# Performance work log

Hardware: AMD Instinct MI355X
Metric: run time of the kernel (lower is better)

Reference implementation:

```python
import jax, jax.numpy as jnp
import numpy as np

B, K, DA, DZ, H = 8, 256, 64, 32, 128
DIR_IN = 2 * DA + 5 + 4 * DZ  # 261
NONE_IN = 5 + 2 * DA + 4 * DZ  # 261
HUGE = 1000000.0


def _init_mlp(key, d_in, h):
    k1, k2, k3 = jax.random.split(key, 3)
    s1 = 1.0 / np.sqrt(d_in)
    s2 = 1.0 / np.sqrt(h)
    return (
        jax.random.uniform(k1, (d_in, h), jnp.float32, -s1, s1), jnp.zeros((h,), jnp.float32),
        jax.random.uniform(k2, (h, h), jnp.float32, -s2, s2), jnp.zeros((h,), jnp.float32),
        jax.random.uniform(k3, (h, 1), jnp.float32, -s2, s2), jnp.zeros((1,), jnp.float32),
    )


def setup_inputs() -> dict:
    key = jax.random.key(0)
    ks = jax.random.split(key, 5)
    agent_feat = jax.random.normal(ks[0], (B, K, DA), jnp.float32)
    z_mean = jax.random.normal(ks[1], (B, K, DZ), jnp.float32)
    z_logvar = jax.random.normal(ks[2], (B, K, DZ), jnp.float32)
    agent_mask = jnp.ones((B, K), jnp.float32)
    W1d, b1d, W2d, b2d, W3d, b3d = _init_mlp(ks[3], DIR_IN, H)
    W1n, b1n, W2n, b2n, W3n, b3n = _init_mlp(ks[4], NONE_IN, H)
    return dict(agent_feat=agent_feat, z_mean=z_mean, z_logvar=z_logvar,
                agent_mask=agent_mask,
                W1d=W1d, b1d=b1d, W2d=W2d, b2d=b2d, W3d=W3d, b3d=b3d,
                W1n=W1n, b1n=b1n, W2n=W2n, b2n=b2n, W3n=W3n, b3n=b3n)


def _mlp(x, W1, b1, W2, b2, W3, b3):
    h = jax.nn.relu(jnp.einsum('bijf,fh->bijh', x, W1) + b1)
    h = jax.nn.relu(jnp.einsum('bijh,hg->bijg', h, W2) + b2)
    return (jnp.einsum('bijh,ho->bijo', h, W3) + b3)[..., 0]  # [B,K,K]


def reference(agent_feat, z_mean, z_logvar, agent_mask,
              W1d, b1d, W2d, b2d, W3d, b3d,
              W1n, b1n, W2n, b2n, W3n, b3n):
    Bv, Kv, Da = agent_feat.shape
    ai = jnp.broadcast_to(agent_feat[:, :, None, :], (Bv, Kv, Kv, Da))
    aj = jnp.broadcast_to(agent_feat[:, None, :, :], (Bv, Kv, Kv, Da))
    Dz = z_mean.shape[-1]
    zi_m = jnp.broadcast_to(z_mean[:, :, None, :], (Bv, Kv, Kv, Dz))
    zj_m = jnp.broadcast_to(z_mean[:, None, :, :], (Bv, Kv, Kv, Dz))
    zi_lv = jnp.broadcast_to(z_logvar[:, :, None, :], (Bv, Kv, Kv, Dz))
    zj_lv = jnp.broadcast_to(z_logvar[:, None, :, :], (Bv, Kv, Kv, Dz))
    rel_pos = aj[..., 0:2] - ai[..., 0:2]
    rel_vel = aj[..., 3:5] - ai[..., 3:5]
    dist = jnp.linalg.norm(rel_pos, axis=-1, keepdims=True)
    geom = jnp.concatenate([rel_pos, rel_vel, dist], axis=-1)  # [B,K,K,5]
    dir_feat = jnp.concatenate([ai, aj, geom, zi_m, zi_lv, zj_m, zj_lv], axis=-1)
    none_feat = jnp.concatenate([geom, ai, aj, zi_m, zi_lv, zj_m, zj_lv], axis=-1)

    e_dir = _mlp(dir_feat, W1d, b1d, W2d, b2d, W3d, b3d)
    e_none = _mlp(none_feat, W1n, b1n, W2n, b2n, W3n, b3n)

    pair_mask = agent_mask[:, :, None] * agent_mask[:, None, :]
    pair_mask = pair_mask * (1.0 - jnp.eye(Kv, dtype=agent_feat.dtype)[None])
    keep = pair_mask > 0.5
    e_dir = jnp.where(keep, e_dir, HUGE)
    e_none = jnp.where(keep, e_none, HUGE)
    e_none = 0.5 * (e_none + jnp.swapaxes(e_none, 1, 2))
    return e_dir, e_none
```

## Files before the change

### kernel.cpp

```cpp
#include <hip/hip_runtime.h>

typedef unsigned short u16;
typedef unsigned int u32;
typedef short s16x8 __attribute__((ext_vector_type(8)));
typedef float f32x4 __attribute__((ext_vector_type(4)));
typedef u32 u32x4 __attribute__((ext_vector_type(4)));

#define UT_D   0u
#define VT_D   524288u
#define UT_N   1048576u
#define VT_N   1572864u
#define W2T_D  2097152u
#define W2T_N  2129920u
#define ERAW   2162688u

__device__ __forceinline__ u16 f2bf(float x) {
  u32 u = __float_as_uint(x);
  return (u16)((u + 0x7FFFu + ((u >> 16) & 1u)) >> 16);
}
__device__ __forceinline__ u32 cvt_pk_bf16(float lo, float hi) {
  u32 r;
  asm("v_cvt_pk_bf16_f32 %0, %1, %2" : "=v"(r) : "v"(lo), "v"(hi));
  return r;
}
__device__ __forceinline__ s16x8 as_frag(u32x4 v) { return __builtin_bit_cast(s16x8, v); }

__global__ __launch_bounds__(256) void k_uv(
    const float* __restrict__ af, const float* __restrict__ zm, const float* __restrict__ zlv,
    const float* __restrict__ W1d, const float* __restrict__ b1d,
    const float* __restrict__ W1n, const float* __restrict__ b1n,
    u16* __restrict__ ws16) {
  const int a0  = blockIdx.x * 8;
  const int mlp = blockIdx.y;
  const int t   = threadIdx.x;
  __shared__ float xs[8][128];
  for (int idx = t; idx < 1024; idx += 256) {
    const int a = idx >> 7, f = idx & 127, ga = a0 + a;
    float v;
    if (f < 64)      v = af[ga*64 + f];
    else if (f < 96) v = zm[ga*32 + (f-64)];
    else             v = zlv[ga*32 + (f-96)];
    xs[a][f] = v;
  }
  __syncthreads();
  const int h = t & 127, half = t >> 7;
  const float* W1 = mlp ? W1n : W1d;
  const int aoff = (mlp ? 5 : 0) + 64*half;
  const int zoff = 69 + 64*half;
  float acc[8];
  #pragma unroll
  for (int a = 0; a < 8; ++a) acc[a] = 0.f;
  #pragma unroll 2
  for (int f = 0; f < 64; f += 4) {
    const float w0 = W1[(aoff+f  )*128 + h];
    const float w1 = W1[(aoff+f+1)*128 + h];
    const float w2 = W1[(aoff+f+2)*128 + h];
    const float w3 = W1[(aoff+f+3)*128 + h];
    #pragma unroll
    for (int a = 0; a < 8; ++a) {
      const f32x4 xv = *(const f32x4*)&xs[a][f];
      acc[a] = fmaf(xv[3], w3, fmaf(xv[2], w2, fmaf(xv[1], w1, fmaf(xv[0], w0, acc[a]))));
    }
  }
  #pragma unroll 2
  for (int f = 64; f < 128; f += 4) {
    const float w0 = W1[(zoff+f  )*128 + h];
    const float w1 = W1[(zoff+f+1)*128 + h];
    const float w2 = W1[(zoff+f+2)*128 + h];
    const float w3 = W1[(zoff+f+3)*128 + h];
    #pragma unroll
    for (int a = 0; a < 8; ++a) {
      const f32x4 xv = *(const f32x4*)&xs[a][f];
      acc[a] = fmaf(xv[3], w3, fmaf(xv[2], w2, fmaf(xv[1], w1, fmaf(xv[0], w0, acc[a]))));
    }
  }
  const float bb = half ? 0.f : (mlp ? b1n[h] : b1d[h]);
  u16 pk[8];
  #pragma unroll
  for (int a = 0; a < 8; ++a) pk[a] = f2bf(acc[a] + bb);
  const int b = a0 >> 8;
  u16* dT = (u16*)((char*)ws16 + (mlp ? (half ? VT_N : UT_N) : (half ? VT_D : UT_D)));
  *(s16x8*)(dT + (b*128 + h)*256 + (a0 & 255)) = *(s16x8*)pk;
}

__global__ __launch_bounds__(256) void k_w2t(
    const float* __restrict__ W2d, const float* __restrict__ W2n, u16* __restrict__ ws16) {
  const int mlp = blockIdx.x, ch = blockIdx.y, t = threadIdx.x;
  const float* W2 = mlp ? W2n : W2d;
  u16* W2s = (u16*)((char*)ws16 + (mlp ? W2T_N : W2T_D));
  int idx = ch*2048 + t;
  #pragma unroll
  for (int rr = 0; rr < 8; ++rr, idx += 256) {
    const int nn = idx >> 7, k = idx & 127;
    const int h = 32*(k>>5) + 16*((k>>2)&1) + 4*((k>>3)&3) + (k&3);
    W2s[nn*128 + k] = f2bf(W2[h*128 + nn]);
  }
}

__global__ __launch_bounds__(256, 2) void k_main(
    const float* __restrict__ af, const float* __restrict__ mask,
    const float* __restrict__ W1d, const float* __restrict__ b2d, const float* __restrict__ W3d, const float* __restrict__ b3d,
    const float* __restrict__ W1n, const float* __restrict__ b2n, const float* __restrict__ W3n, const float* __restrict__ b3n,
    const u16* __restrict__ ws16, float* __restrict__ e_raw, float* __restrict__ out) {
  const int t   = threadIdx.x;
  const int i0  = blockIdx.x * 8;
  const int mlp = blockIdx.y & 1, jc = blockIdx.y >> 1;
  const int b   = blockIdx.z;

  __shared__ u16 w2s[16384];
  __shared__ float b2w3f[2][128];
  __shared__ float maskF[256];

  const u16* W2s_g = (const u16*)((const char*)ws16 + (mlp ? W2T_N : W2T_D));
  {
    const int row = t >> 1, c0 = (t & 1) * 64;
    #pragma unroll
    for (int w = 0; w < 8; ++w) {
      s16x8 v = *(const s16x8*)(W2s_g + row*128 + c0 + w*8);
      const int idx = (row*128 + c0 + w*8) ^ ((row & 7) << 3);
      *(s16x8*)&w2s[idx] = v;
    }
  }
  if (t < 128) b2w3f[0][t] = (mlp ? b2n : b2d)[t];
  else         b2w3f[1][t-128] = (mlp ? W3n : W3d)[t-128];
  maskF[t] = mask[b*256 + t];
  const float b3v = (mlp ? b3n : b3d)[0];

  const int wv = t >> 6, l = t & 63, x = l & 15, g = l >> 4;
  const int xh = x >> 3, xl = x & 7;

  const u16* uT = (const u16*)((const char*)ws16 + (mlp ? UT_N : UT_D));
  const u16* vT = (const u16*)((const char*)ws16 + (mlp ? VT_N : VT_D));
  const float* W1 = mlp ? W1n : W1d;
  const int grow = mlp ? 0 : 128;

  s16x8 Af[8];
  #pragma unroll
  for (int m = 0; m < 8; ++m) {
    u32x4 a = {0u, 0u, 0u, 0u};
    if (g == 0) {
      a = *(const u32x4*)(uT + (b*128 + 16*m + x)*256 + i0);
    } else if (g == 3) {
      const int h = 16*m + x;
      const float w0 = W1[(grow+0)*128 + h], w1 = W1[(grow+1)*128 + h];
      const float w2 = W1[(grow+2)*128 + h], w3 = W1[(grow+3)*128 + h];
      const float w4 = W1[(grow+4)*128 + h];
      a[0] = cvt_pk_bf16(w0, w1); a[1] = cvt_pk_bf16(w2, w3);
      a[2] = cvt_pk_bf16(w4, 0.f); a[3] = 0u;
    }
    Af[m] = __builtin_bit_cast(s16x8, a);
  }

  u32x4 B1u[4];
  #pragma unroll
  for (int n = 0; n < 4; ++n) {
    u32x4 v = {0u, 0u, 0u, 0u};
    if (g == 0) {
      const int il = 2*n + xh;
      v[il >> 1] = (il & 1) ? 0x3F800000u : 0x3F80u;
    } else if (g == 1) {
      v[xl >> 1] = (xl & 1) ? 0x3F800000u : 0x3F80u;
    }
    B1u[n] = v;
  }

  f32x4 aic[4];
  #pragma unroll
  for (int n = 0; n < 4; ++n) {
    const float* ap = af + (b*256 + i0 + 2*n + xh)*64;
    aic[n][0] = ap[0]; aic[n][1] = ap[1]; aic[n][2] = ap[3]; aic[n][3] = ap[4];
  }

  int j0w = jc*128 + wv*8;
  if (g == 1) {
    #pragma unroll
    for (int m = 0; m < 8; ++m)
      Af[m] = *(const s16x8*)(vT + (b*128 + 16*m + x)*256 + j0w);
  }
  float aj0, aj1, aj2, aj3;
  {
    const float* ap = af + (b*256 + j0w + xl)*64;
    aj0 = ap[0]; aj1 = ap[1]; aj2 = ap[3]; aj3 = ap[4];
  }

  __syncthreads();

  const f32x4 zero4 = {0.f, 0.f, 0.f, 0.f};
  #pragma unroll 1
  for (int s = 0; s < 4; ++s, j0w += 32) {
    if (g == 3) {
      #pragma unroll
      for (int n = 0; n < 4; ++n) {
        const float rp0 = aj0 - aic[n][0], rp1 = aj1 - aic[n][1];
        const float rv0 = aj2 - aic[n][2], rv1 = aj3 - aic[n][3];
        const float dist = sqrtf(rp0*rp0 + rp1*rp1);
        u32x4 v;
        v[0] = cvt_pk_bf16(rp0, rp1); v[1] = cvt_pk_bf16(rv0, rv1);
        v[2] = cvt_pk_bf16(dist, 0.f); v[3] = 0u;
        B1u[n] = v;
      }
    }

    u32x4 Bh1[4][4];
    #pragma unroll
    for (int m = 0; m < 8; ++m) {
      #pragma unroll
      for (int n = 0; n < 4; ++n) {
        f32x4 a = __builtin_amdgcn_mfma_f32_16x16x32_bf16(Af[m], as_frag(B1u[n]), zero4, 0, 0, 0);
        const u32 p0 = cvt_pk_bf16(fmaxf(a[0], 0.f), fmaxf(a[1], 0.f));
        const u32 p1 = cvt_pk_bf16(fmaxf(a[2], 0.f), fmaxf(a[3], 0.f));
        if ((m & 1) == 0) { Bh1[m>>1][n][0] = p0; Bh1[m>>1][n][1] = p1; }
        else              { Bh1[m>>1][n][2] = p0; Bh1[m>>1][n][3] = p1; }
      }
    }

    if (s < 3) {
      if (g == 1) {
        #pragma unroll
        for (int m = 0; m < 8; ++m)
          Af[m] = *(const s16x8*)(vT + (b*128 + 16*m + x)*256 + j0w + 32);
      }
      const float* ap = af + (b*256 + j0w + 32 + xl)*64;
      aj0 = ap[0]; aj1 = ap[1]; aj2 = ap[3]; aj3 = ap[4];
    }

    float ep0 = 0.f, ep1 = 0.f, ep2 = 0.f, ep3 = 0.f;
    #pragma unroll
    for (int nq = 0; nq < 4; ++nq) {
      f32x4 acc2[2][4];
      #pragma unroll
      for (int mq = 0; mq < 2; ++mq)
        #pragma unroll
        for (int n = 0; n < 4; ++n) acc2[mq][n] = zero4;
      #pragma unroll
      for (int kk = 0; kk < 4; ++kk) {
        #pragma unroll
        for (int mq = 0; mq < 2; ++mq) {
          const int idx = ((16*(2*nq+mq) + x)*128 + 32*kk + 8*g) ^ ((x & 7) << 3);
          const s16x8 a2 = *(const s16x8*)&w2s[idx];
          #pragma unroll
          for (int n = 0; n < 4; ++n)
            acc2[mq][n] = __builtin_amdgcn_mfma_f32_16x16x32_bf16(a2, as_frag(Bh1[kk][n]), acc2[mq][n], 0, 0, 0);
        }
      }
      #pragma unroll
      for (int mq = 0; mq < 2; ++mq) {
        const int nn0 = 16*(2*nq+mq) + 4*g;
        const f32x4 b2v = *(const f32x4*)&b2w3f[0][nn0];
        const f32x4 w3v = *(const f32x4*)&b2w3f[1][nn0];
        #pragma unroll
        for (int r = 0; r < 4; ++r) {
          ep0 += fmaxf(acc2[mq][0][r] + b2v[r], 0.f) * w3v[r];
          ep1 += fmaxf(acc2[mq][1][r] + b2v[r], 0.f) * w3v[r];
          ep2 += fmaxf(acc2[mq][2][r] + b2v[r], 0.f) * w3v[r];
          ep3 += fmaxf(acc2[mq][3][r] + b2v[r], 0.f) * w3v[r];
        }
      }
    }
    ep0 += __shfl_xor(ep0, 16); ep0 += __shfl_xor(ep0, 32);
    ep1 += __shfl_xor(ep1, 16); ep1 += __shfl_xor(ep1, 32);
    ep2 += __shfl_xor(ep2, 16); ep2 += __shfl_xor(ep2, 32);
    ep3 += __shfl_xor(ep3, 16); ep3 += __shfl_xor(ep3, 32);

    const float es = (g == 0) ? ep0 : (g == 1) ? ep1 : (g == 2) ? ep2 : ep3;
    const int gi = i0 + 2*g + xh, gj = j0w + xl;
    const float e = es + b3v;
    const int off = (b << 16) + (gi << 8) + gj;
    if (mlp == 0) {
      const bool keep = (maskF[gi] * maskF[gj] > 0.5f) && (gi != gj);
      out[off] = keep ? e : 1000000.0f;
    } else {
      e_raw[off] = e;
    }
  }
}

__global__ __launch_bounds__(256) void k_sym(
    const float* __restrict__ e_raw, const float* __restrict__ mask, float* __restrict__ out) {
  const int tp = blockIdx.x, b = blockIdx.y;
  int ti, tj;
  if (tp < 4)      { ti = 0; tj = tp; }
  else if (tp < 7) { ti = 1; tj = tp - 3; }
  else if (tp < 9) { ti = 2; tj = tp - 5; }
  else             { ti = 3; tj = 3; }
  __shared__ float E1[64][65], E2[64][65];
  __shared__ float mI[64], mJ[64];
  const int t = threadIdx.x;
  const int i0 = ti*64, j0 = tj*64, base = b << 16;
  for (int idx = t; idx < 4096; idx += 256) {
    const int r = idx >> 6, c = idx & 63;
    E1[r][c] = e_raw[base + (i0 + r)*256 + j0 + c];
    E2[r][c] = e_raw[base + (j0 + r)*256 + i0 + c];
  }
  if (t < 64)       mI[t] = mask[b*256 + i0 + t];
  else if (t < 128) mJ[t-64] = mask[b*256 + j0 + (t-64)];
  __syncthreads();
  for (int idx = t; idx < 4096; idx += 256) {
    const int r = idx >> 6, c = idx & 63;
    const int i = i0 + r, j = j0 + c;
    float v = 1000000.0f;
    if ((mI[r]*mJ[c] > 0.5f) && (i != j)) v = 0.5f*(E1[r][c] + E2[c][r]);
    out[524288 + base + i*256 + j] = v;
  }
  if (ti != tj) {
    for (int idx = t; idx < 4096; idx += 256) {
      const int r = idx >> 6, c = idx & 63;
      float v = 1000000.0f;
      if (mJ[r]*mI[c] > 0.5f) v = 0.5f*(E2[r][c] + E1[c][r]);
      out[524288 + base + (j0 + r)*256 + i0 + c] = v;
    }
  }
}

extern "C" void kernel_launch(void* const* d_in, const int* in_sizes, int n_in,
                              void* d_out, int out_size, void* d_ws, size_t ws_size,
                              hipStream_t stream) {
  const float* af   = (const float*)d_in[0];
  const float* zm   = (const float*)d_in[1];
  const float* zlv  = (const float*)d_in[2];
  const float* mask = (const float*)d_in[3];
  const float* W1d  = (const float*)d_in[4];
  const float* b1d  = (const float*)d_in[5];
  const float* W2d  = (const float*)d_in[6];
  const float* b2d  = (const float*)d_in[7];
  const float* W3d  = (const float*)d_in[8];
  const float* b3d  = (const float*)d_in[9];
  const float* W1n  = (const float*)d_in[10];
  const float* b1n  = (const float*)d_in[11];
  const float* W2n  = (const float*)d_in[12];
  const float* b2n  = (const float*)d_in[13];
  const float* W3n  = (const float*)d_in[14];
  const float* b3n  = (const float*)d_in[15];

  u16*   ws16  = (u16*)d_ws;
  float* e_raw = (float*)((char*)d_ws + ERAW);
  float* out   = (float*)d_out;

  k_uv <<<dim3(256, 2), 256, 0, stream>>>(af, zm, zlv, W1d, b1d, W1n, b1n, ws16);
  k_w2t<<<dim3(2, 8),   256, 0, stream>>>(W2d, W2n, ws16);
  k_main<<<dim3(32, 4, 8), 256, 0, stream>>>(af, mask, W1d, b2d, W3d, b3d,
                                             W1n, b2n, W3n, b3n, ws16, e_raw, out);
  k_sym<<<dim3(10, 8), 256, 0, stream>>>(e_raw, mask, out);
}
```

Measured before the change: 80.22 us.

## Merge W2 transpose into uv kernel, pad W2 LDS, fold bias into MFMA init

The W2 bf16 transpose kernel becomes an extra block column of the u/v precompute kernel, which removes one kernel launch. In the main kernel the XOR-swizzled W2 shared-memory layout is replaced by a row padding of 136 elements. The b2 bias is used as the initial MFMA accumulator so the epilogue no longer adds it. The layer-2 MFMA loop is also wrapped in s_setprio to raise wave priority. The merged transpose now runs as one serial block per MLP, and the padding uses slightly more LDS.

```diff
diff --git a/kernel.cpp b/kernel.cpp
--- a/kernel.cpp
+++ b/kernel.cpp
@@ -25,14 +25,25 @@
 }
 __device__ __forceinline__ s16x8 as_frag(u32x4 v) { return __builtin_bit_cast(s16x8, v); }
 
-__global__ __launch_bounds__(256) void k_uv(
+__global__ __launch_bounds__(256) void k_uvw(
     const float* __restrict__ af, const float* __restrict__ zm, const float* __restrict__ zlv,
     const float* __restrict__ W1d, const float* __restrict__ b1d,
     const float* __restrict__ W1n, const float* __restrict__ b1n,
+    const float* __restrict__ W2d, const float* __restrict__ W2n,
     u16* __restrict__ ws16) {
-  const int a0  = blockIdx.x * 8;
   const int mlp = blockIdx.y;
   const int t   = threadIdx.x;
+  if (blockIdx.x == 256) {
+    const float* W2 = mlp ? W2n : W2d;
+    u16* W2s = (u16*)((char*)ws16 + (mlp ? W2T_N : W2T_D));
+    for (int idx = t; idx < 16384; idx += 256) {
+      const int nn = idx >> 7, k = idx & 127;
+      const int h = 32*(k>>5) + 16*((k>>2)&1) + 4*((k>>3)&3) + (k&3);
+      W2s[nn*128 + k] = f2bf(W2[h*128 + nn]);
+    }
+    return;
+  }
+  const int a0 = blockIdx.x * 8;
   __shared__ float xs[8][128];
   for (int idx = t; idx < 1024; idx += 256) {
     const int a = idx >> 7, f = idx & 127, ga = a0 + a;
@@ -81,20 +92,6 @@
   const int b = a0 >> 8;
   u16* dT = (u16*)((char*)ws16 + (mlp ? (half ? VT_N : UT_N) : (half ? VT_D : UT_D)));
   *(s16x8*)(dT + (b*128 + h)*256 + (a0 & 255)) = *(s16x8*)pk;
-}
-
-__global__ __launch_bounds__(256) void k_w2t(
-    const float* __restrict__ W2d, const float* __restrict__ W2n, u16* __restrict__ ws16) {
-  const int mlp = blockIdx.x, ch = blockIdx.y, t = threadIdx.x;
-  const float* W2 = mlp ? W2n : W2d;
-  u16* W2s = (u16*)((char*)ws16 + (mlp ? W2T_N : W2T_D));
-  int idx = ch*2048 + t;
-  #pragma unroll
-  for (int rr = 0; rr < 8; ++rr, idx += 256) {
-    const int nn = idx >> 7, k = idx & 127;
-    const int h = 32*(k>>5) + 16*((k>>2)&1) + 4*((k>>3)&3) + (k&3);
-    W2s[nn*128 + k] = f2bf(W2[h*128 + nn]);
-  }
 }
 
 __global__ __launch_bounds__(256, 2) void k_main(
@@ -107,7 +104,7 @@
   const int mlp = blockIdx.y & 1, jc = blockIdx.y >> 1;
   const int b   = blockIdx.z;
 
-  __shared__ u16 w2s[16384];
+  __shared__ u16 w2s[128*136];
   __shared__ float b2w3f[2][128];
   __shared__ float maskF[256];
 
@@ -117,8 +114,7 @@
     #pragma unroll
     for (int w = 0; w < 8; ++w) {
       s16x8 v = *(const s16x8*)(W2s_g + row*128 + c0 + w*8);
-      const int idx = (row*128 + c0 + w*8) ^ ((row & 7) << 3);
-      *(s16x8*)&w2s[idx] = v;
+      *(s16x8*)&w2s[row*136 + c0 + w*8] = v;
     }
   }
   if (t < 128) b2w3f[0][t] = (mlp ? b2n : b2d)[t];
@@ -128,6 +124,7 @@
 
   const int wv = t >> 6, l = t & 63, x = l & 15, g = l >> 4;
   const int xh = x >> 3, xl = x & 7;
+  const int lanebase = 136*x + 8*g;
 
   const u16* uT = (const u16*)((const char*)ws16 + (mlp ? UT_N : UT_D));
   const u16* vT = (const u16*)((const char*)ws16 + (mlp ? VT_N : VT_D));
@@ -225,19 +222,21 @@
     }
 
     float ep0 = 0.f, ep1 = 0.f, ep2 = 0.f, ep3 = 0.f;
+    __builtin_amdgcn_s_setprio(1);
     #pragma unroll
     for (int nq = 0; nq < 4; ++nq) {
       f32x4 acc2[2][4];
       #pragma unroll
-      for (int mq = 0; mq < 2; ++mq)
+      for (int mq = 0; mq < 2; ++mq) {
+        const int w = 2*nq + mq;
+        const f32x4 b2c = *(const f32x4*)&b2w3f[0][16*w + 4*g];
+        const s16x8 a20 = *(const s16x8*)&w2s[lanebase + 2176*w];
         #pragma unroll
-        for (int n = 0; n < 4; ++n) acc2[mq][n] = zero4;
-      #pragma unroll
-      for (int kk = 0; kk < 4; ++kk) {
+        for (int n = 0; n < 4; ++n)
+          acc2[mq][n] = __builtin_amdgcn_mfma_f32_16x16x32_bf16(a20, as_frag(Bh1[0][n]), b2c, 0, 0, 0);
         #pragma unroll
-        for (int mq = 0; mq < 2; ++mq) {
-          const int idx = ((16*(2*nq+mq) + x)*128 + 32*kk + 8*g) ^ ((x & 7) << 3);
-          const s16x8 a2 = *(const s16x8*)&w2s[idx];
+        for (int kk = 1; kk < 4; ++kk) {
+          const s16x8 a2 = *(const s16x8*)&w2s[lanebase + 2176*w + 32*kk];
           #pragma unroll
           for (int n = 0; n < 4; ++n)
             acc2[mq][n] = __builtin_amdgcn_mfma_f32_16x16x32_bf16(a2, as_frag(Bh1[kk][n]), acc2[mq][n], 0, 0, 0);
@@ -245,18 +244,18 @@
       }
       #pragma unroll
       for (int mq = 0; mq < 2; ++mq) {
-        const int nn0 = 16*(2*nq+mq) + 4*g;
-        const f32x4 b2v = *(const f32x4*)&b2w3f[0][nn0];
-        const f32x4 w3v = *(const f32x4*)&b2w3f[1][nn0];
+        const int w = 2*nq + mq;
+        const f32x4 w3v = *(const f32x4*)&b2w3f[1][16*w + 4*g];
         #pragma unroll
         for (int r = 0; r < 4; ++r) {
-          ep0 += fmaxf(acc2[mq][0][r] + b2v[r], 0.f) * w3v[r];
-          ep1 += fmaxf(acc2[mq][1][r] + b2v[r], 0.f) * w3v[r];
-          ep2 += fmaxf(acc2[mq][2][r] + b2v[r], 0.f) * w3v[r];
-          ep3 += fmaxf(acc2[mq][3][r] + b2v[r], 0.f) * w3v[r];
+          ep0 += fmaxf(acc2[mq][0][r], 0.f) * w3v[r];
+          ep1 += fmaxf(acc2[mq][1][r], 0.f) * w3v[r];
+          ep2 += fmaxf(acc2[mq][2][r], 0.f) * w3v[r];
+          ep3 += fmaxf(acc2[mq][3][r], 0.f) * w3v[r];
         }
       }
     }
+    __builtin_amdgcn_s_setprio(0);
     ep0 += __shfl_xor(ep0, 16); ep0 += __shfl_xor(ep0, 32);
     ep1 += __shfl_xor(ep1, 16); ep1 += __shfl_xor(ep1, 32);
     ep2 += __shfl_xor(ep2, 16); ep2 += __shfl_xor(ep2, 32);
@@ -336,8 +335,7 @@
   float* e_raw = (float*)((char*)d_ws + ERAW);
   float* out   = (float*)d_out;
 
-  k_uv <<<dim3(256, 2), 256, 0, stream>>>(af, zm, zlv, W1d, b1d, W1n, b1n, ws16);
-  k_w2t<<<dim3(2, 8),   256, 0, stream>>>(W2d, W2n, ws16);
+  k_uvw<<<dim3(257, 2), 256, 0, stream>>>(af, zm, zlv, W1d, b1d, W1n, b1n, W2d, W2n, ws16);
   k_main<<<dim3(32, 4, 8), 256, 0, stream>>>(af, mask, W1d, b2d, W3d, b3d,
                                              W1n, b2n, W3n, b3n, ws16, e_raw, out);
   k_sym<<<dim3(10, 8), 256, 0, stream>>>(e_raw, mask, out);
```

Measured after the change: 77.98 us. -2.8%, faster.
